# Optimization experiments

Hardware: AMD Instinct MI355X
Metric: run time of the kernel (lower is better)

The kernel has to match this reference:

```python
import jax, jax.numpy as jnp
import numpy as np

WINDOW = (8, 8)
NUM_HEADS = 12


def setup_inputs() -> dict:
    key = jax.random.key(0)
    k0, k1, k2 = jax.random.split(key, 3)
    B_, H, W, C = 8, 64, 64, 768
    x = jax.random.normal(k0, (B_, H * W, C), dtype=jnp.float32)
    qkv_w = jax.random.normal(k1, (3 * C, C), dtype=jnp.float32) * 0.02
    qkv_b = jnp.zeros((3 * C,), dtype=jnp.float32)
    proj_w = jax.random.normal(k2, (C, C), dtype=jnp.float32) * 0.02
    proj_b = jnp.zeros((C,), dtype=jnp.float32)
    return {"x": x, "qkv_w": qkv_w, "qkv_b": qkv_b,
            "proj_w": proj_w, "proj_b": proj_b, "H": H, "W": W}


def reference(x, qkv_w, qkv_b, proj_w, proj_b, H, W):
    ws0, ws1 = WINDOW
    nh = NUM_HEADS
    B_, N, C = x.shape
    hd = C // nh
    scale = hd ** (-0.5)

    x = x.reshape(B_, H, W, C)
    # pad bottom/right so H, W divisible by window size (static Python ints)
    pad_b = (ws0 - H % ws0) % ws0
    pad_r = (ws1 - W % ws1) % ws1
    x = jnp.pad(x, ((0, 0), (0, pad_b), (0, pad_r), (0, 0)))
    Hp, Wp = H + pad_b, W + pad_r

    # window partition: (B, Hp, Wp, C) -> (B*nW, ws0*ws1, C)
    xw = (x.reshape(B_, Hp // ws0, ws0, Wp // ws1, ws1, C)
            .transpose(0, 1, 3, 2, 4, 5)
            .reshape(-1, ws0 * ws1, C))
    Bw, Nw = xw.shape[0], xw.shape[1]

    # fused qkv projection
    qkv = xw @ qkv_w.T + qkv_b                       # (Bw, Nw, 3C)
    qkv = qkv.reshape(Bw, Nw, 3, nh, hd).transpose(2, 0, 3, 1, 4)
    q, k, v = qkv[0], qkv[1], qkv[2]                 # (Bw, nh, Nw, hd)

    attn = jax.nn.softmax((q * scale) @ jnp.swapaxes(k, -2, -1), axis=-1)
    out = (attn @ v).transpose(0, 2, 1, 3).reshape(Bw, Nw, C)
    out = out @ proj_w.T + proj_b

    # window reverse: (B*nW, ws0*ws1, C) -> (B, Hp, Wp, C)
    out = (out.reshape(B_, Hp // ws0, Wp // ws1, ws0, ws1, C)
              .transpose(0, 1, 3, 2, 4, 5)
              .reshape(B_, Hp, Wp, C))
    out = out[:, :H, :W, :]
    return out.reshape(B_, H * W, C)
```

## Files before the change

### kernel.cpp

```cpp
#include <hip/hip_runtime.h>
#include <stdint.h>

typedef __attribute__((ext_vector_type(8))) __bf16 bf16x8;
typedef __attribute__((ext_vector_type(4))) float f32x4;
typedef __attribute__((ext_vector_type(8))) unsigned short u16x8;
typedef __attribute__((ext_vector_type(2))) unsigned int u32x2;

__device__ __forceinline__ unsigned short f2bf(float f) {
  union { float f; unsigned u; } v; v.f = f;
  return (unsigned short)((v.u + 0x7FFFu + ((v.u >> 16) & 1u)) >> 16);
}

__device__ __forceinline__ void gload16(const void* g, void* l) {
  __builtin_amdgcn_global_load_lds(
      (const __attribute__((address_space(1))) void*)g,
      (__attribute__((address_space(3))) void*)l, 16, 0, 0);
}

__global__ __launch_bounds__(256) void pack_x_kernel(const float* __restrict__ x,
                                                     unsigned short* __restrict__ xw) {
  int idx = blockIdx.x * 256 + threadIdx.x;
  int m = idx / 96;
  int p = idx - m * 96;
  int win = m >> 6, tok = m & 63;
  int b = win >> 6, wh = (win >> 3) & 7, ww = win & 7;
  int r = tok >> 3, c = tok & 7;
  size_t xoff = ((size_t)b * 4096 + (wh * 8 + r) * 64 + (ww * 8 + c)) * 768 + p * 8;
  const float* src = x + xoff;
  u16x8 o;
#pragma unroll
  for (int j = 0; j < 8; ++j) o[j] = f2bf(src[j]);
  *(u16x8*)(xw + (size_t)m * 768 + p * 8) = o;
}

__global__ __launch_bounds__(256) void pack_w_kernel(const float* __restrict__ qkvw,
                                                     const float* __restrict__ projw,
                                                     unsigned short* __restrict__ wq,
                                                     unsigned short* __restrict__ wp) {
  int idx = blockIdx.x * 256 + threadIdx.x;
  const float* src;
  unsigned short* dst;
  if (idx < 221184) { src = qkvw + (size_t)idx * 8; dst = wq + (size_t)idx * 8; }
  else { int i2 = idx - 221184; src = projw + (size_t)i2 * 8; dst = wp + (size_t)i2 * 8; }
  u16x8 o;
#pragma unroll
  for (int j = 0; j < 8; ++j) o[j] = f2bf(src[j]);
  *(u16x8*)dst = o;
}

template <int N, bool PROJ>
__global__ __launch_bounds__(256, 3) void gemm128_kernel(
    const unsigned short* __restrict__ A, const unsigned short* __restrict__ Bm,
    const float* __restrict__ bias, void* __restrict__ Cout) {
  constexpr int K = 768;
  constexpr int NT = K / 32;
  constexpr int NBN = N / 128;
  __shared__ char smem[49152];

  const int tid = threadIdx.x;
  const int wave = tid >> 6;
  const int lane = tid & 63;
  const int wmr = wave >> 1;
  const int wnc = wave & 1;

  const int cpx = gridDim.x >> 3;
  const int bid = (blockIdx.x & 7) * cpx + (blockIdx.x >> 3);
  const int tm = (bid / NBN) * 128;
  const int tn = (bid % NBN) * 128;

  const int srow0 = wave * 16 + (lane >> 2);
  const int sgl = ((lane & 3) ^ ((lane >> 3) & 3)) * 8;
  const unsigned short* gA0 = A + (size_t)(tm + srow0) * K + sgl;
  const unsigned short* gA1 = A + (size_t)(tm + 64 + srow0) * K + sgl;
  const unsigned short* gB0 = Bm + (size_t)(tn + srow0) * K + sgl;
  const unsigned short* gB1 = Bm + (size_t)(tn + 64 + srow0) * K + sgl;
  const int ldsW = wave * 1024;

#define STAGE(s, slot) do {                                        \
    char* d_ = smem + (slot) * 16384;                              \
    gload16(gA0 + (s) * 32, d_ + ldsW);                            \
    gload16(gA1 + (s) * 32, d_ + 4096 + ldsW);                     \
    gload16(gB0 + (s) * 32, d_ + 8192 + ldsW);                     \
    gload16(gB1 + (s) * 32, d_ + 12288 + ldsW);                    \
  } while (0)

  const int lrow = lane & 15;
  const int pgb = (((lane >> 4) ^ ((lane >> 1) & 3)) << 4);

  STAGE(0, 0);
  STAGE(1, 1);
  asm volatile("s_waitcnt vmcnt(4)" ::: "memory");
  asm volatile("s_barrier" ::: "memory");

  f32x4 acc[4][4] = {};

  bf16x8 a0[2], b[4];
  {
    const char* aB = smem + (wmr * 64 + lrow) * 64 + pgb;
    const char* bB = smem + 8192 + (wnc * 64 + lrow) * 64 + pgb;
#pragma unroll
    for (int mi = 0; mi < 2; ++mi) a0[mi] = *(const bf16x8*)(aB + mi * 1024);
#pragma unroll
    for (int ni = 0; ni < 4; ++ni) b[ni] = *(const bf16x8*)(bB + ni * 1024);
  }

#pragma unroll
  for (int t = 0; t < NT; ++t) {
    const char* cb = smem + (t % 3) * 16384;
    const char* aB = cb + (wmr * 64 + lrow) * 64 + pgb;

    if (t + 2 < NT) STAGE(t + 2, (t + 2) % 3);
    bf16x8 a1[2];
#pragma unroll
    for (int mi = 0; mi < 2; ++mi)
      a1[mi] = *(const bf16x8*)(aB + (2 + mi) * 1024);

    __builtin_amdgcn_s_setprio(1);
#pragma unroll
    for (int mi = 0; mi < 2; ++mi)
#pragma unroll
      for (int ni = 0; ni < 4; ++ni)
        acc[mi][ni] = __builtin_amdgcn_mfma_f32_16x16x32_bf16(b[ni], a0[mi], acc[mi][ni], 0, 0, 0);
    __builtin_amdgcn_s_setprio(0);

    if (t + 2 < NT)
      asm volatile("s_waitcnt vmcnt(4)" ::: "memory");
    else if (t == NT - 2)
      asm volatile("s_waitcnt vmcnt(0)" ::: "memory");
    if (t + 1 < NT)
      asm volatile("s_barrier" ::: "memory");

    bf16x8 a0n[2], bn[4];
    if (t + 1 < NT) {
      const char* nb = smem + ((t + 1) % 3) * 16384;
      const char* aN = nb + (wmr * 64 + lrow) * 64 + pgb;
      const char* bN = nb + 8192 + (wnc * 64 + lrow) * 64 + pgb;
#pragma unroll
      for (int mi = 0; mi < 2; ++mi) a0n[mi] = *(const bf16x8*)(aN + mi * 1024);
#pragma unroll
      for (int ni = 0; ni < 4; ++ni) bn[ni] = *(const bf16x8*)(bN + ni * 1024);
    }

    __builtin_amdgcn_s_setprio(1);
#pragma unroll
    for (int mi = 0; mi < 2; ++mi)
#pragma unroll
      for (int ni = 0; ni < 4; ++ni)
        acc[2 + mi][ni] = __builtin_amdgcn_mfma_f32_16x16x32_bf16(b[ni], a1[mi], acc[2 + mi][ni], 0, 0, 0);
    __builtin_amdgcn_s_setprio(0);

#pragma unroll
    for (int i = 0; i < 2; ++i) a0[i] = a0n[i];
#pragma unroll
    for (int i = 0; i < 4; ++i) b[i] = bn[i];
  }
#undef STAGE

  const int erow = tm + wmr * 64 + (lane & 15);
  const int ecol = tn + wnc * 64 + ((lane >> 4) << 2);
  if constexpr (!PROJ) {
    unsigned short* C = (unsigned short*)Cout;
#pragma unroll
    for (int ni = 0; ni < 4; ++ni) {
      const int col0 = ecol + ni * 16;
      const f32x4 bv = *(const f32x4*)&bias[col0];
#pragma unroll
      for (int mi = 0; mi < 4; ++mi) {
        f32x4 v = acc[mi][ni];
        u32x2 pk;
        pk.x = (unsigned)f2bf(v[0] + bv[0]) | ((unsigned)f2bf(v[1] + bv[1]) << 16);
        pk.y = (unsigned)f2bf(v[2] + bv[2]) | ((unsigned)f2bf(v[3] + bv[3]) << 16);
        *(u32x2*)(C + (size_t)(erow + mi * 16) * N + col0) = pk;
      }
    }
  } else {
    float* out = (float*)Cout;
    f32x4 bv[4];
#pragma unroll
    for (int ni = 0; ni < 4; ++ni) bv[ni] = *(const f32x4*)&bias[ecol + ni * 16];
#pragma unroll
    for (int mi = 0; mi < 4; ++mi) {
      int m = erow + mi * 16;
      int win = m >> 6, tok = m & 63;
      int bb = win >> 6, wh = (win >> 3) & 7, ww = win & 7;
      int rr = tok >> 3, cc = tok & 7;
      float* op = out + ((size_t)bb * 4096 + (wh * 8 + rr) * 64 + (ww * 8 + cc)) * 768;
#pragma unroll
      for (int ni = 0; ni < 4; ++ni) {
        f32x4 o = acc[mi][ni] + bv[ni];
        *(f32x4*)(op + ecol + ni * 16) = o;
      }
    }
  }
}

__global__ __launch_bounds__(64) void attn_kernel(const unsigned short* __restrict__ qkv,
                                                  unsigned short* __restrict__ attnout) {
  __shared__ unsigned short sQ[64 * 64];
  __shared__ unsigned short sK[64 * 64];
  __shared__ unsigned short sVT[64 * 64];
  const int lane = threadIdx.x;
  const int win = blockIdx.x / 12;
  const int head = blockIdx.x - win * 12;
  const size_t row0 = (size_t)win * 64;
  const int qoff = head * 64, koff = 768 + head * 64, voff = 1536 + head * 64;

#pragma unroll
  for (int i = 0; i < 8; ++i) {
    int e = lane + i * 64;
    int row = e >> 3, cb = (e & 7) * 8;
    gload16(qkv + (row0 + row) * 2304 + qoff + cb, (char*)sQ + i * 1024);
    gload16(qkv + (row0 + row) * 2304 + koff + cb, (char*)sK + i * 1024);
  }
  {
    const unsigned short* gv = qkv + (row0 + lane) * 2304 + voff;
#pragma unroll
    for (int j = 0; j < 8; ++j) {
      u16x8 v = *(const u16x8*)(gv + j * 8);
#pragma unroll
      for (int d = 0; d < 8; ++d) sVT[(j * 8 + d) * 64 + lane] = v[d];
    }
  }
  __syncthreads();

  const int lrow = lane & 15;
  const int lkb = (lane >> 4) * 8;

  f32x4 s[4][4] = {};
#pragma unroll
  for (int ks = 0; ks < 2; ++ks) {
    bf16x8 qf[4], kf[4];
#pragma unroll
    for (int mi = 0; mi < 4; ++mi) qf[mi] = *(const bf16x8*)&sQ[(mi * 16 + lrow) * 64 + ks * 32 + lkb];
#pragma unroll
    for (int ni = 0; ni < 4; ++ni) kf[ni] = *(const bf16x8*)&sK[(ni * 16 + lrow) * 64 + ks * 32 + lkb];
#pragma unroll
    for (int mi = 0; mi < 4; ++mi)
#pragma unroll
      for (int ni = 0; ni < 4; ++ni)
        s[mi][ni] = __builtin_amdgcn_mfma_f32_16x16x32_bf16(qf[mi], kf[ni], s[mi][ni], 0, 0, 0);
  }

  float p[4][4][4];
#pragma unroll
  for (int mi = 0; mi < 4; ++mi) {
#pragma unroll
    for (int r = 0; r < 4; ++r) {
      float v0 = s[mi][0][r] * 0.125f, v1 = s[mi][1][r] * 0.125f;
      float v2 = s[mi][2][r] * 0.125f, v3 = s[mi][3][r] * 0.125f;
      float mx = fmaxf(fmaxf(v0, v1), fmaxf(v2, v3));
      mx = fmaxf(mx, __shfl_xor(mx, 1));
      mx = fmaxf(mx, __shfl_xor(mx, 2));
      mx = fmaxf(mx, __shfl_xor(mx, 4));
      mx = fmaxf(mx, __shfl_xor(mx, 8));
      float e0 = __expf(v0 - mx), e1 = __expf(v1 - mx);
      float e2 = __expf(v2 - mx), e3 = __expf(v3 - mx);
      float sm = e0 + e1 + e2 + e3;
      sm += __shfl_xor(sm, 1);
      sm += __shfl_xor(sm, 2);
      sm += __shfl_xor(sm, 4);
      sm += __shfl_xor(sm, 8);
      float inv = 1.0f / sm;
      p[mi][0][r] = e0 * inv; p[mi][1][r] = e1 * inv;
      p[mi][2][r] = e2 * inv; p[mi][3][r] = e3 * inv;
    }
  }

  __syncthreads();
#pragma unroll
  for (int mi = 0; mi < 4; ++mi)
#pragma unroll
    for (int ni = 0; ni < 4; ++ni)
#pragma unroll
      for (int r = 0; r < 4; ++r)
        sK[(mi * 16 + (lane >> 4) * 4 + r) * 64 + ni * 16 + lrow] = f2bf(p[mi][ni][r]);
  __syncthreads();

  f32x4 o[4][4] = {};
#pragma unroll
  for (int ks = 0; ks < 2; ++ks) {
    bf16x8 pf[4], vf[4];
#pragma unroll
    for (int mi = 0; mi < 4; ++mi) pf[mi] = *(const bf16x8*)&sK[(mi * 16 + lrow) * 64 + ks * 32 + lkb];
#pragma unroll
    for (int ni = 0; ni < 4; ++ni) vf[ni] = *(const bf16x8*)&sVT[(ni * 16 + lrow) * 64 + ks * 32 + lkb];
#pragma unroll
    for (int mi = 0; mi < 4; ++mi)
#pragma unroll
      for (int ni = 0; ni < 4; ++ni)
        o[mi][ni] = __builtin_amdgcn_mfma_f32_16x16x32_bf16(pf[mi], vf[ni], o[mi][ni], 0, 0, 0);
  }

#pragma unroll
  for (int mi = 0; mi < 4; ++mi)
#pragma unroll
    for (int ni = 0; ni < 4; ++ni) {
      int col = head * 64 + ni * 16 + lrow;
#pragma unroll
      for (int r = 0; r < 4; ++r) {
        int trow = mi * 16 + (lane >> 4) * 4 + r;
        attnout[(row0 + trow) * 768 + col] = f2bf(o[mi][ni][r]);
      }
    }
}

extern "C" void kernel_launch(void* const* d_in, const int* in_sizes, int n_in,
                              void* d_out, int out_size, void* d_ws, size_t ws_size,
                              hipStream_t stream) {
  (void)in_sizes; (void)n_in; (void)out_size; (void)ws_size;
  const float* x = (const float*)d_in[0];
  const float* qkv_w = (const float*)d_in[1];
  const float* qkv_b = (const float*)d_in[2];
  const float* proj_w = (const float*)d_in[3];
  const float* proj_b = (const float*)d_in[4];
  float* out = (float*)d_out;

  char* ws = (char*)d_ws;
  unsigned short* xw   = (unsigned short*)(ws);
  unsigned short* qkvB = (unsigned short*)(ws + 50331648);
  unsigned short* wq   = (unsigned short*)(ws + 50331648 + 150994944);
  unsigned short* wp   = (unsigned short*)(ws + 50331648 + 150994944 + 3538944);

  pack_x_kernel<<<12288, 256, 0, stream>>>(x, xw);
  pack_w_kernel<<<1152, 256, 0, stream>>>(qkv_w, proj_w, wq, wp);
  gemm128_kernel<2304, false><<<4608, 256, 0, stream>>>(xw, wq, qkv_b, qkvB);
  attn_kernel<<<6144, 64, 0, stream>>>(qkvB, xw);
  gemm128_kernel<768, true><<<1536, 256, 0, stream>>>(xw, wp, proj_b, out);
}
```

Baseline: 296.5 us.

## Widen GEMM tiles to 128x256 with double-buffered LDS staging

Both GEMMs now use a 128x256 output tile per block instead of 128x128. Each wave computes all 128 rows for its own 64-column strip, which halves the block count and raises per-block arithmetic intensity on the shared A tile. The three-slot LDS pipeline with a two-stage prefetch is replaced by a two-slot double buffer that waits for all loads (vmcnt(0)) every iteration. This trades less latency hiding and more accumulator registers for more data reuse.

```diff
diff --git a/kernel.cpp b/kernel.cpp
--- a/kernel.cpp
+++ b/kernel.cpp
@@ -49,115 +49,94 @@
 }
 
 template <int N, bool PROJ>
-__global__ __launch_bounds__(256, 3) void gemm128_kernel(
+__global__ __launch_bounds__(256, 3) void gemm_kernel(
     const unsigned short* __restrict__ A, const unsigned short* __restrict__ Bm,
     const float* __restrict__ bias, void* __restrict__ Cout) {
   constexpr int K = 768;
   constexpr int NT = K / 32;
-  constexpr int NBN = N / 128;
+  constexpr int NBN = N / 256;
   __shared__ char smem[49152];
 
   const int tid = threadIdx.x;
   const int wave = tid >> 6;
   const int lane = tid & 63;
-  const int wmr = wave >> 1;
-  const int wnc = wave & 1;
 
   const int cpx = gridDim.x >> 3;
   const int bid = (blockIdx.x & 7) * cpx + (blockIdx.x >> 3);
   const int tm = (bid / NBN) * 128;
-  const int tn = (bid % NBN) * 128;
-
-  const int srow0 = wave * 16 + (lane >> 2);
-  const int sgl = ((lane & 3) ^ ((lane >> 3) & 3)) * 8;
-  const unsigned short* gA0 = A + (size_t)(tm + srow0) * K + sgl;
-  const unsigned short* gA1 = A + (size_t)(tm + 64 + srow0) * K + sgl;
-  const unsigned short* gB0 = Bm + (size_t)(tn + srow0) * K + sgl;
-  const unsigned short* gB1 = Bm + (size_t)(tn + 64 + srow0) * K + sgl;
+  const int tn = (bid % NBN) * 256;
+
+  const int srow = tid >> 2;
+  const int sgl = ((tid & 3) ^ ((tid >> 3) & 3)) * 8;
+  const unsigned short* gA0 = A + (size_t)(tm + srow) * K + sgl;
+  const unsigned short* gA1 = A + (size_t)(tm + 64 + srow) * K + sgl;
+  const unsigned short* gB0 = Bm + (size_t)(tn + srow) * K + sgl;
+  const unsigned short* gB1 = Bm + (size_t)(tn + 64 + srow) * K + sgl;
+  const unsigned short* gB2 = Bm + (size_t)(tn + 128 + srow) * K + sgl;
+  const unsigned short* gB3 = Bm + (size_t)(tn + 192 + srow) * K + sgl;
   const int ldsW = wave * 1024;
 
 #define STAGE(s, slot) do {                                        \
-    char* d_ = smem + (slot) * 16384;                              \
+    char* d_ = smem + (slot) * 24576;                              \
     gload16(gA0 + (s) * 32, d_ + ldsW);                            \
     gload16(gA1 + (s) * 32, d_ + 4096 + ldsW);                     \
     gload16(gB0 + (s) * 32, d_ + 8192 + ldsW);                     \
     gload16(gB1 + (s) * 32, d_ + 12288 + ldsW);                    \
+    gload16(gB2 + (s) * 32, d_ + 16384 + ldsW);                    \
+    gload16(gB3 + (s) * 32, d_ + 20480 + ldsW);                    \
   } while (0)
 
   const int lrow = lane & 15;
   const int pgb = (((lane >> 4) ^ ((lane >> 1) & 3)) << 4);
 
   STAGE(0, 0);
-  STAGE(1, 1);
-  asm volatile("s_waitcnt vmcnt(4)" ::: "memory");
+  asm volatile("s_waitcnt vmcnt(0)" ::: "memory");
   asm volatile("s_barrier" ::: "memory");
 
-  f32x4 acc[4][4] = {};
-
-  bf16x8 a0[2], b[4];
-  {
-    const char* aB = smem + (wmr * 64 + lrow) * 64 + pgb;
-    const char* bB = smem + 8192 + (wnc * 64 + lrow) * 64 + pgb;
-#pragma unroll
-    for (int mi = 0; mi < 2; ++mi) a0[mi] = *(const bf16x8*)(aB + mi * 1024);
+  f32x4 acc[8][4] = {};
+
+#pragma unroll
+  for (int t = 0; t < NT; ++t) {
+    if (t + 1 < NT) STAGE(t + 1, (t + 1) & 1);
+
+    const char* sb = smem + (t & 1) * 24576;
+    const char* aB = sb + lrow * 64 + pgb;
+    const char* bB = sb + 8192 + (wave * 64 + lrow) * 64 + pgb;
+
+    bf16x8 b[4], a[4];
 #pragma unroll
     for (int ni = 0; ni < 4; ++ni) b[ni] = *(const bf16x8*)(bB + ni * 1024);
-  }
-
-#pragma unroll
-  for (int t = 0; t < NT; ++t) {
-    const char* cb = smem + (t % 3) * 16384;
-    const char* aB = cb + (wmr * 64 + lrow) * 64 + pgb;
-
-    if (t + 2 < NT) STAGE(t + 2, (t + 2) % 3);
-    bf16x8 a1[2];
-#pragma unroll
-    for (int mi = 0; mi < 2; ++mi)
-      a1[mi] = *(const bf16x8*)(aB + (2 + mi) * 1024);
+#pragma unroll
+    for (int mi = 0; mi < 4; ++mi) a[mi] = *(const bf16x8*)(aB + mi * 1024);
 
     __builtin_amdgcn_s_setprio(1);
 #pragma unroll
-    for (int mi = 0; mi < 2; ++mi)
+    for (int mi = 0; mi < 4; ++mi)
 #pragma unroll
       for (int ni = 0; ni < 4; ++ni)
-        acc[mi][ni] = __builtin_amdgcn_mfma_f32_16x16x32_bf16(b[ni], a0[mi], acc[mi][ni], 0, 0, 0);
+        acc[mi][ni] = __builtin_amdgcn_mfma_f32_16x16x32_bf16(b[ni], a[mi], acc[mi][ni], 0, 0, 0);
     __builtin_amdgcn_s_setprio(0);
 
-    if (t + 2 < NT)
-      asm volatile("s_waitcnt vmcnt(4)" ::: "memory");
-    else if (t == NT - 2)
+#pragma unroll
+    for (int mi = 0; mi < 4; ++mi) a[mi] = *(const bf16x8*)(aB + (4 + mi) * 1024);
+
+    __builtin_amdgcn_s_setprio(1);
+#pragma unroll
+    for (int mi = 0; mi < 4; ++mi)
+#pragma unroll
+      for (int ni = 0; ni < 4; ++ni)
+        acc[4 + mi][ni] = __builtin_amdgcn_mfma_f32_16x16x32_bf16(b[ni], a[mi], acc[4 + mi][ni], 0, 0, 0);
+    __builtin_amdgcn_s_setprio(0);
+
+    if (t + 1 < NT) {
       asm volatile("s_waitcnt vmcnt(0)" ::: "memory");
-    if (t + 1 < NT)
       asm volatile("s_barrier" ::: "memory");
-
-    bf16x8 a0n[2], bn[4];
-    if (t + 1 < NT) {
-      const char* nb = smem + ((t + 1) % 3) * 16384;
-      const char* aN = nb + (wmr * 64 + lrow) * 64 + pgb;
-      const char* bN = nb + 8192 + (wnc * 64 + lrow) * 64 + pgb;
-#pragma unroll
-      for (int mi = 0; mi < 2; ++mi) a0n[mi] = *(const bf16x8*)(aN + mi * 1024);
-#pragma unroll
-      for (int ni = 0; ni < 4; ++ni) bn[ni] = *(const bf16x8*)(bN + ni * 1024);
-    }
-
-    __builtin_amdgcn_s_setprio(1);
-#pragma unroll
-    for (int mi = 0; mi < 2; ++mi)
-#pragma unroll
-      for (int ni = 0; ni < 4; ++ni)
-        acc[2 + mi][ni] = __builtin_amdgcn_mfma_f32_16x16x32_bf16(b[ni], a1[mi], acc[2 + mi][ni], 0, 0, 0);
-    __builtin_amdgcn_s_setprio(0);
-
-#pragma unroll
-    for (int i = 0; i < 2; ++i) a0[i] = a0n[i];
-#pragma unroll
-    for (int i = 0; i < 4; ++i) b[i] = bn[i];
+    }
   }
 #undef STAGE
 
-  const int erow = tm + wmr * 64 + (lane & 15);
-  const int ecol = tn + wnc * 64 + ((lane >> 4) << 2);
+  const int erow = tm + (lane & 15);
+  const int ecol = tn + wave * 64 + ((lane >> 4) << 2);
   if constexpr (!PROJ) {
     unsigned short* C = (unsigned short*)Cout;
 #pragma unroll
@@ -165,7 +144,7 @@
       const int col0 = ecol + ni * 16;
       const f32x4 bv = *(const f32x4*)&bias[col0];
 #pragma unroll
-      for (int mi = 0; mi < 4; ++mi) {
+      for (int mi = 0; mi < 8; ++mi) {
         f32x4 v = acc[mi][ni];
         u32x2 pk;
         pk.x = (unsigned)f2bf(v[0] + bv[0]) | ((unsigned)f2bf(v[1] + bv[1]) << 16);
@@ -179,7 +158,7 @@
 #pragma unroll
     for (int ni = 0; ni < 4; ++ni) bv[ni] = *(const f32x4*)&bias[ecol + ni * 16];
 #pragma unroll
-    for (int mi = 0; mi < 4; ++mi) {
+    for (int mi = 0; mi < 8; ++mi) {
       int m = erow + mi * 16;
       int win = m >> 6, tok = m & 63;
       int bb = win >> 6, wh = (win >> 3) & 7, ww = win & 7;
@@ -323,7 +302,7 @@
 
   pack_x_kernel<<<12288, 256, 0, stream>>>(x, xw);
   pack_w_kernel<<<1152, 256, 0, stream>>>(qkv_w, proj_w, wq, wp);
-  gemm128_kernel<2304, false><<<4608, 256, 0, stream>>>(xw, wq, qkv_b, qkvB);
+  gemm_kernel<2304, false><<<2304, 256, 0, stream>>>(xw, wq, qkv_b, qkvB);
   attn_kernel<<<6144, 64, 0, stream>>>(qkvB, xw);
-  gemm128_kernel<768, true><<<1536, 256, 0, stream>>>(xw, wp, proj_b, out);
-}
+  gemm_kernel<768, true><<<768, 256, 0, stream>>>(xw, wp, proj_b, out);
+}
```

New measurement: 545.2 us. 1.84x slower.
